# Performance work log

Measured on AMD Instinct MI355X. Metric: run time of the kernel, lower is better.

Reference implementation:

```python
import jax, jax.numpy as jnp
import numpy as np

N, P, D, C = 8192, 512, 2, 4   # queries, coeff grid points, spatial dim, num coefficients
HA = 32                        # attention_net hidden
HP, CP = 32, 16                # pointswise_mlp hidden / output
HG = 256                       # green_function_net hidden


def setup_inputs() -> dict:
    key = jax.random.key(0)
    ks = jax.random.split(key, 16)
    g = lambda k, shp, s: jax.random.normal(k, shp, dtype=jnp.float32) * s
    return {
        "r": g(ks[0], (N, 2 * D), 1.0),
        "r_prime": g(ks[1], (N, 2 * D), 1.0),
        "coeff_x": g(ks[2], (P, D), 1.0),
        "coeff_y": g(ks[3], (P, C), 1.0),
        # attention_net MLP (no bias): concat(q,k)=4 -> 32 -> 32 -> 1
        "Wa1": g(ks[4], (2 * D, HA), 0.5),
        "Wa2": g(ks[5], (HA, HA), 1.0 / np.sqrt(HA)),
        "Wa3": g(ks[6], (HA, 1), 1.0 / np.sqrt(HA)),
        # pointswise_mlp: C -> 32 -> 16
        "Wp1": g(ks[7], (C, HP), 0.5), "bp1": jnp.zeros((HP,), jnp.float32),
        "Wp2": g(ks[8], (HP, CP), 1.0 / np.sqrt(HP)), "bp2": jnp.zeros((CP,), jnp.float32),
        # green_function_net: 4+4+16=24 -> 256 -> 256 -> 1 (exp at the end)
        "Wg1": g(ks[9], (2 * D + 2 * D + CP, HG), 1.0 / np.sqrt(24.0)), "bg1": jnp.zeros((HG,), jnp.float32),
        "Wg2": g(ks[10], (HG, HG), 1.0 / np.sqrt(HG)), "bg2": jnp.zeros((HG,), jnp.float32),
        "Wg3": g(ks[11], (HG, 1), 0.1 / np.sqrt(HG)), "bg3": jnp.zeros((1,), jnp.float32),
    }


def reference(r, r_prime, coeff_x, coeff_y,
              Wa1, Wa2, Wa3, Wp1, bp1, Wp2, bp2,
              Wg1, bg1, Wg2, bg2, Wg3, bg3):
    # --- CoefficientNet: pairwise MLP attention over the coefficient grid ---
    q = r[:, :D]  # (N, 2) spatial position only
    # first layer of attn MLP on concat([q, k]) split into q- and k- parts
    h = jax.nn.relu(q @ Wa1[:D][None if False else slice(None)]  # (N, HA)
                    [..., :] [..., :]  # no-op for readability
                    if False else (q @ Wa1[:D])[:, None, :] + (coeff_x @ Wa1[D:])[None, :, :])  # (N, P, HA)
    h = jax.nn.relu(h @ Wa2)                     # (N, P, HA)
    logits = (h @ Wa3)[..., 0]                   # (N, P)
    attn = jax.nn.softmax(logits, axis=-1)       # (N, P)
    attn_out = attn @ coeff_y                    # (N, C)
    c = jax.nn.relu(attn_out @ Wp1 + bp1) @ Wp2 + bp2  # (N, CP)
    # --- GreenFunctionNet ---
    x = jnp.concatenate([r, r_prime, c], axis=-1)       # (N, 24)
    g1 = jax.nn.relu(x @ Wg1 + bg1)
    g2 = jax.nn.relu(g1 @ Wg2 + bg2)
    return jnp.exp(g2 @ Wg3 + bg3)                      # (N, 1)
```

## Files before the change

kernel.cpp:

```cpp
#include <hip/hip_runtime.h>
#include <math.h>

#define N_ 8192
#define P_ 512

typedef __fp16 half8  __attribute__((ext_vector_type(8)));
typedef __fp16 half2t __attribute__((ext_vector_type(2)));
typedef float  floatx16 __attribute__((ext_vector_type(16)));

union H8 { half8 v; half2t h2[4]; };

static __device__ __forceinline__ half2t pk2(float a, float b) {
    return __builtin_amdgcn_cvt_pkrtz(a, b);
}

#define HP_OFF  17408
#define XS_OFF  21760
#define WP2_OFF 25088

__global__ __launch_bounds__(512, 4) void k_fused(
    const float* __restrict__ r,
    const float* __restrict__ rp,
    const float* __restrict__ coeff_x,
    const float* __restrict__ coeff_y,
    const float* __restrict__ Wa1,
    const float* __restrict__ Wa2,
    const float* __restrict__ Wa3,
    const float* __restrict__ Wp1,
    const float* __restrict__ bp1,
    const float* __restrict__ Wp2,
    const float* __restrict__ bp2,
    const float* __restrict__ Wg1,
    const float* __restrict__ bg1,
    const float* __restrict__ Wg2,
    const float* __restrict__ bg2,
    const float* __restrict__ Wg3,
    const float* __restrict__ bg3,
    float* __restrict__ out)
{
    __shared__ __align__(16) unsigned char reg0[49152];
    __shared__ __align__(16) float4 cyS[512];
    __shared__ float sA[8][32];
    __shared__ float aoA[4][8][32];
    __shared__ float aoS[32][4];
    __shared__ float sredS[32];

    const int tid  = threadIdx.x;
    const int n0   = blockIdx.x * 32;
    const int lane = tid & 63;
    const int wv   = tid >> 6;
    const int j32  = lane & 31;
    const int hl   = lane >> 5;
    const int k0g  = hl * 8;

    {
        const float2 cx = ((const float2*)coeff_x)[tid];
        half2t* wrow = (half2t*)(reg0 + tid * 96);
#pragma unroll
        for (int q = 0; q < 16; ++q) {
            const float b0 = cx.x * Wa1[64 + 2*q]     + cx.y * Wa1[96 + 2*q];
            const float b1 = cx.x * Wa1[64 + 2*q + 1] + cx.y * Wa1[96 + 2*q + 1];
            wrow[q] = pk2(b0, b1);
        }
        cyS[tid] = ((const float4*)coeff_y)[tid];
    }

    H8 anh1, anh2;
    {
        const float2 rv = ((const float2*)r)[2 * (n0 + j32)];
#pragma unroll
        for (int q = 0; q < 4; ++q) {
            const int k1 = k0g + 2*q, k2 = 16 + k0g + 2*q;
            anh1.h2[q] = pk2(rv.x*Wa1[k1]   + rv.y*Wa1[32+k1],
                             rv.x*Wa1[k1+1] + rv.y*Wa1[32+k1+1]);
            anh2.h2[q] = pk2(rv.x*Wa1[k2]   + rv.y*Wa1[32+k2],
                             rv.x*Wa1[k2+1] + rv.y*Wa1[32+k2+1]);
        }
    }
    H8 af1, af2;
#pragma unroll
    for (int q = 0; q < 4; ++q) {
        af1.h2[q] = pk2(Wa2[(k0g + 2*q)     * 32 + j32],
                        Wa2[(k0g + 2*q + 1) * 32 + j32]);
        af2.h2[q] = pk2(Wa2[(16 + k0g + 2*q)     * 32 + j32],
                        Wa2[(16 + k0g + 2*q + 1) * 32 + j32]);
    }
    half2t w3h[8];
#pragma unroll
    for (int q = 0; q < 8; ++q) {
        const int r0 = ((2*q) & 3) + 8*(q >> 1) + 4*hl;
        w3h[q] = pk2(Wa3[r0], Wa3[r0 + 1]);
    }

    __syncthreads();

    const half2t zero2 = pk2(0.f, 0.f);
    float s = 0.0f, aox = 0.f, aoy = 0.f, aoz = 0.f, aow = 0.f;

#pragma unroll 2
    for (int pl = 0; pl < 64; ++pl) {
        const int ploc = wv * 64 + pl;
        const half2t* rowq = (const half2t*)(reg0 + ploc * 96) + hl * 4;

        H8 bf1, bf2;
#pragma unroll
        for (int q = 0; q < 4; ++q) {
            bf1.h2[q] = __builtin_elementwise_max(anh1.h2[q] + rowq[q],     zero2);
            bf2.h2[q] = __builtin_elementwise_max(anh2.h2[q] + rowq[8 + q], zero2);
        }

        floatx16 zc = {};
        floatx16 acc = __builtin_amdgcn_mfma_f32_32x32x16_f16(af1.v, bf1.v, zc, 0, 0, 0);
        acc = __builtin_amdgcn_mfma_f32_32x32x16_f16(af2.v, bf2.v, acc, 0, 0, 0);

        float d0, d1, d2, d3;
        {
            half2t z0 = __builtin_elementwise_max(pk2(acc[0],  acc[1]),  zero2);
            half2t z1 = __builtin_elementwise_max(pk2(acc[2],  acc[3]),  zero2);
            half2t z2 = __builtin_elementwise_max(pk2(acc[4],  acc[5]),  zero2);
            half2t z3 = __builtin_elementwise_max(pk2(acc[6],  acc[7]),  zero2);
            half2t z4 = __builtin_elementwise_max(pk2(acc[8],  acc[9]),  zero2);
            half2t z5 = __builtin_elementwise_max(pk2(acc[10], acc[11]), zero2);
            half2t z6 = __builtin_elementwise_max(pk2(acc[12], acc[13]), zero2);
            half2t z7 = __builtin_elementwise_max(pk2(acc[14], acc[15]), zero2);
            d0 = __builtin_amdgcn_fdot2(z1, w3h[1], __builtin_amdgcn_fdot2(z0, w3h[0], 0.f, false), false);
            d1 = __builtin_amdgcn_fdot2(z3, w3h[3], __builtin_amdgcn_fdot2(z2, w3h[2], 0.f, false), false);
            d2 = __builtin_amdgcn_fdot2(z5, w3h[5], __builtin_amdgcn_fdot2(z4, w3h[4], 0.f, false), false);
            d3 = __builtin_amdgcn_fdot2(z7, w3h[7], __builtin_amdgcn_fdot2(z6, w3h[6], 0.f, false), false);
        }
        float dot = (d0 + d1) + (d2 + d3);
        dot += __shfl_xor(dot, 32);

        const float e = __expf(dot);
        const float4 cyv = cyS[ploc];
        s   += e;
        aox += e * cyv.x;
        aoy += e * cyv.y;
        aoz += e * cyv.z;
        aow += e * cyv.w;
    }

    const int jcol = (wv << 5) + j32;
    const int nB = tid & 31;
    const int iB = tid >> 5;

    float wg2f[64];
#pragma unroll
    for (int kk = 0; kk < 8; ++kk)
#pragma unroll
        for (int t = 0; t < 4; ++t) {
            const int kb = kk*16 + hl*8 + 2*t;
            wg2f[kk*8 + 2*t]     = Wg2[kb*256 + jcol];
            wg2f[kk*8 + 2*t + 1] = Wg2[(kb+1)*256 + jcol];
        }
    float wg1f[8], wg1g[8];
    const float bg1v = bg1[jcol];
#pragma unroll
    for (int q = 0; q < 4; ++q) {
        wg1f[2*q]   = Wg1[(k0g + 2*q)*256 + jcol];
        wg1f[2*q+1] = Wg1[(k0g + 2*q + 1)*256 + jcol];
        wg1g[2*q]   = Wg1[(16 + 2*q)*256 + jcol];
        wg1g[2*q+1] = Wg1[(17 + 2*q)*256 + jcol];
    }
    const float wp2pre = Wp2[tid];
    float xpre = 0.f;
    if (tid < 256) {
        const int nn = tid >> 3, k = tid & 7;
        xpre = (k < 4) ? r[(n0+nn)*4 + k] : rp[(n0+nn)*4 + k - 4];
    }
    float wpb[2], wpA[2][4];
#pragma unroll
    for (int rep = 0; rep < 2; ++rep) {
        const int i = iB + rep*16;
        wpb[rep]    = bp1[i];
        wpA[rep][0] = Wp1[i];
        wpA[rep][1] = Wp1[32 + i];
        wpA[rep][2] = Wp1[64 + i];
        wpA[rep][3] = Wp1[96 + i];
    }
    const float bp2v = bp2[iB];
    const float bg2v = bg2[jcol];
    const float w3vv = Wg3[jcol];
    const float bg3v = bg3[0];

    H8 wPre[8];
#pragma unroll
    for (int kk = 0; kk < 8; ++kk)
#pragma unroll
        for (int t = 0; t < 4; ++t)
            wPre[kk].h2[t] = pk2(wg2f[kk*8 + 2*t], wg2f[kk*8 + 2*t + 1]);
    H8 wb1p, wb2p;
#pragma unroll
    for (int q = 0; q < 4; ++q) {
        wb1p.h2[q] = pk2(wg1f[2*q], wg1f[2*q+1]);
        wb2p.h2[q] = (hl == 0) ? pk2(wg1g[2*q], wg1g[2*q+1]) : pk2(0.f, 0.f);
    }

    if (lane < 32) {
        sA[wv][lane]      = s;
        aoA[0][wv][lane]  = aox;
        aoA[1][wv][lane]  = aoy;
        aoA[2][wv][lane]  = aoz;
        aoA[3][wv][lane]  = aow;
    }
    __syncthreads();

    float* wp2S = (float*)(reg0 + WP2_OFF);
    wp2S[tid] = wp2pre;
    if (tid < 160) {
        const int g5 = tid >> 5, c = tid & 31;
        if (g5 == 0) {
            float S = 0.f;
#pragma unroll
            for (int w = 0; w < 8; ++w) S += sA[w][c];
            sredS[c] = S;
        } else {
            float A = 0.f;
#pragma unroll
            for (int w = 0; w < 8; ++w) A += aoA[g5-1][w][c];
            aoS[c][g5-1] = A;
        }
    }
    __syncthreads();

    float* hpS = (float*)(reg0 + HP_OFF);
    float* xS  = (float*)(reg0 + XS_OFF);

    if (tid < 256) {
        const int nn = tid >> 3, k = tid & 7;
        xS[nn*25 + k] = xpre;
    }
    {
        const float inv = 1.0f / sredS[nB];
        const float a0 = aoS[nB][0], a1 = aoS[nB][1], a2 = aoS[nB][2], a3 = aoS[nB][3];
#pragma unroll
        for (int rep = 0; rep < 2; ++rep) {
            float t = a0*wpA[rep][0] + a1*wpA[rep][1]
                    + a2*wpA[rep][2] + a3*wpA[rep][3];
            float a = wpb[rep] + inv * t;
            hpS[nB*33 + iB + rep*16] = fmaxf(a, 0.0f);
        }
    }
    __syncthreads();

    {
        float a = bp2v;
#pragma unroll
        for (int i = 0; i < 32; ++i) a += hpS[nB*33 + i] * wp2S[i*16 + iB];
        xS[nB*25 + 8 + iB] = a;
    }
    __syncthreads();

    __fp16* g1S = (__fp16*)reg0;

    {
        H8 xa1, xa2;
        const float* xrow = xS + j32 * 25;
#pragma unroll
        for (int q = 0; q < 4; ++q) {
            xa1.h2[q] = pk2(xrow[k0g + 2*q], xrow[k0g + 2*q + 1]);
            xa2.h2[q] = (hl == 0) ? pk2(xrow[16 + 2*q], xrow[16 + 2*q + 1])
                                  : pk2(0.f, 0.f);
        }
        floatx16 g1acc = {};
        g1acc = __builtin_amdgcn_mfma_f32_32x32x16_f16(xa1.v, wb1p.v, g1acc, 0, 0, 0);
        g1acc = __builtin_amdgcn_mfma_f32_32x32x16_f16(xa2.v, wb2p.v, g1acc, 0, 0, 0);

#pragma unroll
        for (int i = 0; i < 16; ++i) {
            const int row = (i & 3) + 8*(i >> 2) + 4*hl;
            g1S[row*264 + jcol] = (__fp16)fmaxf(g1acc[i] + bg1v, 0.0f);
        }
    }
    __syncthreads();

    {
        floatx16 acc2 = {};
        const __fp16* arow = g1S + j32 * 264;

        float l2[32];
#pragma unroll
        for (int q = 0; q < 4; ++q)
#pragma unroll
            for (int t = 0; t < 4; ++t) {
                const int kb = (8 + q)*16 + hl*8 + 2*t;
                l2[q*8 + 2*t]     = Wg2[kb*256 + jcol];
                l2[q*8 + 2*t + 1] = Wg2[(kb+1)*256 + jcol];
            }
#pragma unroll
        for (int q = 0; q < 4; ++q) {
            H8 af;
            af.v = *(const half8*)(arow + q*16 + hl*8);
            acc2 = __builtin_amdgcn_mfma_f32_32x32x16_f16(af.v, wPre[q].v, acc2, 0, 0, 0);
        }

        float l3[32];
#pragma unroll
        for (int q = 0; q < 4; ++q)
#pragma unroll
            for (int t = 0; t < 4; ++t) {
                const int kb = (12 + q)*16 + hl*8 + 2*t;
                l3[q*8 + 2*t]     = Wg2[kb*256 + jcol];
                l3[q*8 + 2*t + 1] = Wg2[(kb+1)*256 + jcol];
            }
#pragma unroll
        for (int q = 0; q < 4; ++q) {
            H8 af;
            af.v = *(const half8*)(arow + (4 + q)*16 + hl*8);
            acc2 = __builtin_amdgcn_mfma_f32_32x32x16_f16(af.v, wPre[4+q].v, acc2, 0, 0, 0);
        }

        H8 w2[4];
#pragma unroll
        for (int q = 0; q < 4; ++q)
#pragma unroll
            for (int t = 0; t < 4; ++t)
                w2[q].h2[t] = pk2(l2[q*8 + 2*t], l2[q*8 + 2*t + 1]);
#pragma unroll
        for (int q = 0; q < 4; ++q) {
            H8 af;
            af.v = *(const half8*)(arow + (8 + q)*16 + hl*8);
            acc2 = __builtin_amdgcn_mfma_f32_32x32x16_f16(af.v, w2[q].v, acc2, 0, 0, 0);
        }

        H8 w3[4];
#pragma unroll
        for (int q = 0; q < 4; ++q)
#pragma unroll
            for (int t = 0; t < 4; ++t)
                w3[q].h2[t] = pk2(l3[q*8 + 2*t], l3[q*8 + 2*t + 1]);
#pragma unroll
        for (int q = 0; q < 4; ++q) {
            H8 af;
            af.v = *(const half8*)(arow + (12 + q)*16 + hl*8);
            acc2 = __builtin_amdgcn_mfma_f32_32x32x16_f16(af.v, w3[q].v, acc2, 0, 0, 0);
        }

        float part[16];
#pragma unroll
        for (int i = 0; i < 16; ++i)
            part[i] = fmaxf(acc2[i] + bg2v, 0.0f) * w3vv;
#pragma unroll
        for (int off = 1; off <= 16; off <<= 1) {
#pragma unroll
            for (int i = 0; i < 16; ++i) part[i] += __shfl_xor(part[i], off);
        }
        float* redS = &sA[0][0];
        if ((lane & 31) == 0) {
#pragma unroll
            for (int i = 0; i < 16; ++i) {
                const int row = (i & 3) + 8*(i >> 2) + 4*hl;
                redS[wv*32 + row] = part[i];
            }
        }
        __syncthreads();

        if (tid < 32) {
            float v = bg3v;
#pragma unroll
            for (int w = 0; w < 8; ++w) v += redS[w*32 + tid];
            out[n0 + tid] = __expf(v);
        }
    }
}

extern "C" void kernel_launch(void* const* d_in, const int* in_sizes, int n_in,
                              void* d_out, int out_size, void* d_ws, size_t ws_size,
                              hipStream_t stream)
{
    const float* r   = (const float*)d_in[0];
    const float* rp  = (const float*)d_in[1];
    const float* cx  = (const float*)d_in[2];
    const float* cy  = (const float*)d_in[3];
    const float* Wa1 = (const float*)d_in[4];
    const float* Wa2 = (const float*)d_in[5];
    const float* Wa3 = (const float*)d_in[6];
    const float* Wp1 = (const float*)d_in[7];
    const float* bp1 = (const float*)d_in[8];
    const float* Wp2 = (const float*)d_in[9];
    const float* bp2 = (const float*)d_in[10];
    const float* Wg1 = (const float*)d_in[11];
    const float* bg1 = (const float*)d_in[12];
    const float* Wg2 = (const float*)d_in[13];
    const float* bg2 = (const float*)d_in[14];
    const float* Wg3 = (const float*)d_in[15];
    const float* bg3 = (const float*)d_in[16];

    hipLaunchKernelGGL(k_fused, dim3(N_/32), dim3(512), 0, stream,
                       r, rp, cx, cy, Wa1, Wa2, Wa3, Wp1, bp1, Wp2, bp2,
                       Wg1, bg1, Wg2, bg2, Wg3, bg3, (float*)d_out);
}
```

Measured before the change: 126.4 us.

## Software-pipeline attention LDS loads, cut Wg2 register prefetch, transpose Wp2 in LDS

The attention loop now double-buffers its per-point LDS row loads, fetching the next point's data before the current point's MFMA/softmax work so LDS latency overlaps compute. The Wg2 register preload before the reduction is halved (4 tiles instead of 8), and the remaining tiles are loaded in a rolling fashion during the second-layer GEMM, which reduces register pressure. Wp2 is stored transposed with padding in shared memory to change the access pattern in the small pointwise MLP. The tradeoff is that less global-load latency is hidden before the GEMM.

```diff
diff --git a/kernel.cpp b/kernel.cpp
--- a/kernel.cpp
+++ b/kernel.cpp
@@ -14,9 +14,9 @@
     return __builtin_amdgcn_cvt_pkrtz(a, b);
 }
 
-#define HP_OFF  17408
-#define XS_OFF  21760
-#define WP2_OFF 25088
+#define HP_OFF   17408
+#define XS_OFF   21760
+#define WP2T_OFF 25088
 
 __global__ __launch_bounds__(512, 4) void k_fused(
     const float* __restrict__ r,
@@ -97,18 +97,15 @@
     const half2t zero2 = pk2(0.f, 0.f);
     float s = 0.0f, aox = 0.f, aoy = 0.f, aoz = 0.f, aow = 0.f;
 
-#pragma unroll 2
-    for (int pl = 0; pl < 64; ++pl) {
-        const int ploc = wv * 64 + pl;
-        const half2t* rowq = (const half2t*)(reg0 + ploc * 96) + hl * 4;
-
+    const unsigned char* wbase = reg0 + (wv * 64) * 96 + hl * 16;
+
+    auto ATT = [&](const int ploc, const H8 rq1, const H8 rq2) {
         H8 bf1, bf2;
 #pragma unroll
         for (int q = 0; q < 4; ++q) {
-            bf1.h2[q] = __builtin_elementwise_max(anh1.h2[q] + rowq[q],     zero2);
-            bf2.h2[q] = __builtin_elementwise_max(anh2.h2[q] + rowq[8 + q], zero2);
-        }
-
+            bf1.h2[q] = __builtin_elementwise_max(anh1.h2[q] + rq1.h2[q], zero2);
+            bf2.h2[q] = __builtin_elementwise_max(anh2.h2[q] + rq2.h2[q], zero2);
+        }
         floatx16 zc = {};
         floatx16 acc = __builtin_amdgcn_mfma_f32_32x32x16_f16(af1.v, bf1.v, zc, 0, 0, 0);
         acc = __builtin_amdgcn_mfma_f32_32x32x16_f16(af2.v, bf2.v, acc, 0, 0, 0);
@@ -138,20 +135,36 @@
         aoy += e * cyv.y;
         aoz += e * cyv.z;
         aow += e * cyv.w;
+    };
+
+    H8 rA1, rA2, rB1, rB2;
+    rA1.v = *(const half8*)(wbase);
+    rA2.v = *(const half8*)(wbase + 32);
+
+    for (int pl = 0; pl < 64; pl += 2) {
+        const int pb = pl + 1;
+        rB1.v = *(const half8*)(wbase + pb*96);
+        rB2.v = *(const half8*)(wbase + pb*96 + 32);
+        ATT(wv*64 + pl, rA1, rA2);
+
+        const int pn = (pl + 2) & 63;
+        rA1.v = *(const half8*)(wbase + pn*96);
+        rA2.v = *(const half8*)(wbase + pn*96 + 32);
+        ATT(wv*64 + pb, rB1, rB2);
     }
 
     const int jcol = (wv << 5) + j32;
     const int nB = tid & 31;
     const int iB = tid >> 5;
 
-    float wg2f[64];
-#pragma unroll
-    for (int kk = 0; kk < 8; ++kk)
+    float wg2p[32];
+#pragma unroll
+    for (int q = 0; q < 4; ++q)
 #pragma unroll
         for (int t = 0; t < 4; ++t) {
-            const int kb = kk*16 + hl*8 + 2*t;
-            wg2f[kk*8 + 2*t]     = Wg2[kb*256 + jcol];
-            wg2f[kk*8 + 2*t + 1] = Wg2[(kb+1)*256 + jcol];
+            const int kb = q*16 + hl*8 + 2*t;
+            wg2p[q*8 + 2*t]     = Wg2[kb*256 + jcol];
+            wg2p[q*8 + 2*t + 1] = Wg2[(kb+1)*256 + jcol];
         }
     float wg1f[8], wg1g[8];
     const float bg1v = bg1[jcol];
@@ -183,12 +196,12 @@
     const float w3vv = Wg3[jcol];
     const float bg3v = bg3[0];
 
-    H8 wPre[8];
-#pragma unroll
-    for (int kk = 0; kk < 8; ++kk)
+    H8 wPre[4];
+#pragma unroll
+    for (int q = 0; q < 4; ++q)
 #pragma unroll
         for (int t = 0; t < 4; ++t)
-            wPre[kk].h2[t] = pk2(wg2f[kk*8 + 2*t], wg2f[kk*8 + 2*t + 1]);
+            wPre[q].h2[t] = pk2(wg2p[q*8 + 2*t], wg2p[q*8 + 2*t + 1]);
     H8 wb1p, wb2p;
 #pragma unroll
     for (int q = 0; q < 4; ++q) {
@@ -205,8 +218,8 @@
     }
     __syncthreads();
 
-    float* wp2S = (float*)(reg0 + WP2_OFF);
-    wp2S[tid] = wp2pre;
+    float* wp2T = (float*)(reg0 + WP2T_OFF);
+    wp2T[(tid & 15) * 33 + (tid >> 4)] = wp2pre;
     if (tid < 160) {
         const int g5 = tid >> 5, c = tid & 31;
         if (g5 == 0) {
@@ -246,7 +259,7 @@
     {
         float a = bp2v;
 #pragma unroll
-        for (int i = 0; i < 32; ++i) a += hpS[nB*33 + i] * wp2S[i*16 + iB];
+        for (int i = 0; i < 32; ++i) a += hpS[nB*33 + i] * wp2T[iB*33 + i];
         xS[nB*25 + 8 + iB] = a;
     }
     __syncthreads();
@@ -278,6 +291,28 @@
         floatx16 acc2 = {};
         const __fp16* arow = g1S + j32 * 264;
 
+        float l1[32];
+#pragma unroll
+        for (int q = 0; q < 4; ++q)
+#pragma unroll
+            for (int t = 0; t < 4; ++t) {
+                const int kb = (4 + q)*16 + hl*8 + 2*t;
+                l1[q*8 + 2*t]     = Wg2[kb*256 + jcol];
+                l1[q*8 + 2*t + 1] = Wg2[(kb+1)*256 + jcol];
+            }
+#pragma unroll
+        for (int q = 0; q < 4; ++q) {
+            H8 af;
+            af.v = *(const half8*)(arow + q*16 + hl*8);
+            acc2 = __builtin_amdgcn_mfma_f32_32x32x16_f16(af.v, wPre[q].v, acc2, 0, 0, 0);
+        }
+
+        H8 w1[4];
+#pragma unroll
+        for (int q = 0; q < 4; ++q)
+#pragma unroll
+            for (int t = 0; t < 4; ++t)
+                w1[q].h2[t] = pk2(l1[q*8 + 2*t], l1[q*8 + 2*t + 1]);
         float l2[32];
 #pragma unroll
         for (int q = 0; q < 4; ++q)
@@ -290,10 +325,16 @@
 #pragma unroll
         for (int q = 0; q < 4; ++q) {
             H8 af;
-            af.v = *(const half8*)(arow + q*16 + hl*8);
-            acc2 = __builtin_amdgcn_mfma_f32_32x32x16_f16(af.v, wPre[q].v, acc2, 0, 0, 0);
-        }
-
+            af.v = *(const half8*)(arow + (4 + q)*16 + hl*8);
+            acc2 = __builtin_amdgcn_mfma_f32_32x32x16_f16(af.v, w1[q].v, acc2, 0, 0, 0);
+        }
+
+        H8 w2[4];
+#pragma unroll
+        for (int q = 0; q < 4; ++q)
+#pragma unroll
+            for (int t = 0; t < 4; ++t)
+                w2[q].h2[t] = pk2(l2[q*8 + 2*t], l2[q*8 + 2*t + 1]);
         float l3[32];
 #pragma unroll
         for (int q = 0; q < 4; ++q)
@@ -303,19 +344,6 @@
                 l3[q*8 + 2*t]     = Wg2[kb*256 + jcol];
                 l3[q*8 + 2*t + 1] = Wg2[(kb+1)*256 + jcol];
             }
-#pragma unroll
-        for (int q = 0; q < 4; ++q) {
-            H8 af;
-            af.v = *(const half8*)(arow + (4 + q)*16 + hl*8);
-            acc2 = __builtin_amdgcn_mfma_f32_32x32x16_f16(af.v, wPre[4+q].v, acc2, 0, 0, 0);
-        }
-
-        H8 w2[4];
-#pragma unroll
-        for (int q = 0; q < 4; ++q)
-#pragma unroll
-            for (int t = 0; t < 4; ++t)
-                w2[q].h2[t] = pk2(l2[q*8 + 2*t], l2[q*8 + 2*t + 1]);
 #pragma unroll
         for (int q = 0; q < 4; ++q) {
             H8 af;
```

After: 110.2 us. 12.8% less time.
